# Kernel optimization log

Hardware: AMD Instinct MI355X
Metric: run time of the kernel (lower is better)

Reference implementation:

```python
import jax, jax.numpy as jnp
import numpy as np

MAX_W, MIN_W = 120, 24


def setup_inputs() -> dict:
    key = jax.random.key(0)
    ks = jax.random.split(key, 11)
    B, S, D, H = 2, 2048, 1024, 16
    hd = D // H
    s = 1.0 / float(np.sqrt(D))
    return {
        "x": jax.random.normal(ks[0], (B, S, D), jnp.float32),
        "alpha": jnp.float32(0.1),
        "Wq": jax.random.normal(ks[1], (D, D), jnp.float32) * s,
        "bq": jnp.zeros((D,), jnp.float32),
        "Wk": jax.random.normal(ks[2], (D, D), jnp.float32) * s,
        "bk": jnp.zeros((D,), jnp.float32),
        "Wv": jax.random.normal(ks[3], (D, D), jnp.float32) * s,
        "bv": jnp.zeros((D,), jnp.float32),
        "W_o": jax.random.normal(ks[4], (H, hd, hd), jnp.float32),
        "Wfc": jax.random.normal(ks[5], (D, D), jnp.float32) * s,
        "bfc": jnp.zeros((D,), jnp.float32),
    }


def reference(x, alpha, Wq, bq, Wk, bk, Wv, bv, W_o, Wfc, bfc):
    B, S, D = x.shape
    H, hd, _ = W_o.shape
    # --- dynamic window size (step==0 path of the module) ---
    fluct = jnp.abs(x[:, -1] - x[:, -2])            # [B, D]
    a = jax.nn.sigmoid(alpha)
    ewma_prev = fluct[0, 0]                          # step==0: ewma_prev = fluct_step_value
    signal = a * fluct.mean() + (1.0 - a) * ewma_prev
    scale = jax.nn.sigmoid(signal)
    w = jnp.floor(MIN_W + (MAX_W - MIN_W) * scale).astype(jnp.int32)  # int() truncation
    half = w // 2
    # --- projections ---
    q = (x @ Wq + bq).reshape(B, S, H, hd).transpose(0, 2, 1, 3)  # [B,H,S,hd]
    k = (x @ Wk + bk).reshape(B, S, H, hd).transpose(0, 2, 1, 3)
    v = (x @ Wv + bv).reshape(B, S, H, hd).transpose(0, 2, 1, 3)
    inv_sqrt = 1.0 / float(np.sqrt(hd))
    scores = jnp.einsum('bhqd,bhkd->bhqk', q, k) * inv_sqrt       # [B,H,S,S]
    # banded window mask: allowed iff i - w//2 <= j <= i + w//2
    idx = jnp.arange(S)
    band = jnp.abs(idx[:, None] - idx[None, :]) <= half            # [S,S]
    scores = jnp.where(band[None, None], scores, -1e30)
    attn = jax.nn.softmax(scores, axis=-1)
    out = jnp.einsum('bhqk,bhkd->bhqd', attn, v)                   # [B,H,S,hd]
    out = jnp.einsum('bhqd,hdk->bhqk', out, W_o)                   # per-head output matmul
    out = out.transpose(0, 2, 1, 3).reshape(B, S, D)
    return out @ Wfc + bfc
```

## Files before the change

### kernel.cpp

```cpp
#include <hip/hip_runtime.h>
#include <hip/hip_bf16.h>
#include <stdint.h>
#include <stddef.h>

#define S_LEN 2048
#define DMODEL 1024
#define NHEAD 16
#define HDIM 64
#define BATCH 2
#define MROWS (BATCH * S_LEN)
#define QKV_LD 3072

typedef unsigned short u16;
typedef __attribute__((ext_vector_type(8))) short bf16x8;
typedef __attribute__((ext_vector_type(4))) float f32x4;

__device__ inline u16 f32_to_bf16(float f) {
  union { float f; unsigned int u; } v; v.f = f;
  unsigned int u = v.u;
  unsigned int r = (u + 0x7fffu + ((u >> 16) & 1u)) >> 16;
  return (u16)r;
}

__device__ inline void gload16(const u16* g, u16* l) {
  __builtin_amdgcn_global_load_lds(
      (const __attribute__((address_space(1))) unsigned int*)g,
      (__attribute__((address_space(3))) unsigned int*)l, 16, 0, 0);
}

__global__ __launch_bounds__(256) void conv_x_bf16(const float* __restrict__ x,
                                                   u16* __restrict__ xb,
                                                   const float* __restrict__ alpha,
                                                   int* __restrict__ halfw) {
  if (blockIdx.x == 2048) {
    __shared__ float red[4];
    int tid = threadIdx.x;
    float s = 0.f;
    for (int i = tid; i < BATCH * DMODEL; i += 256) {
      int b = i >> 10, d = i & 1023;
      size_t base = (size_t)b * S_LEN * DMODEL + d;
      float f1 = x[base + (size_t)(S_LEN - 1) * DMODEL];
      float f0 = x[base + (size_t)(S_LEN - 2) * DMODEL];
      s += fabsf(f1 - f0);
    }
#pragma unroll
    for (int m = 32; m >= 1; m >>= 1) s += __shfl_xor(s, m, 64);
    if ((tid & 63) == 0) red[tid >> 6] = s;
    __syncthreads();
    if (tid == 0) {
      float total = red[0] + red[1] + red[2] + red[3];
      float mean = total / (float)(BATCH * DMODEL);
      float e1 = x[(size_t)(S_LEN - 1) * DMODEL];
      float e0 = x[(size_t)(S_LEN - 2) * DMODEL];
      float ew = fabsf(e1 - e0);
      float a = 1.f / (1.f + expf(-alpha[0]));
      float sig = a * mean + (1.f - a) * ew;
      float scale = 1.f / (1.f + expf(-sig));
      int wv = (int)floorf(24.f + 96.f * scale);
      *halfw = wv >> 1;
    }
    return;
  }
  size_t i = ((size_t)blockIdx.x * 256 + threadIdx.x) * 8;
  float4 v0 = *(const float4*)(x + i);
  float4 v1 = *(const float4*)(x + i + 4);
  bf16x8 r;
  r[0] = (short)f32_to_bf16(v0.x); r[1] = (short)f32_to_bf16(v0.y);
  r[2] = (short)f32_to_bf16(v0.z); r[3] = (short)f32_to_bf16(v0.w);
  r[4] = (short)f32_to_bf16(v1.x); r[5] = (short)f32_to_bf16(v1.y);
  r[6] = (short)f32_to_bf16(v1.z); r[7] = (short)f32_to_bf16(v1.w);
  *(bf16x8*)(xb + i) = r;
}

__global__ __launch_bounds__(256) void transpose_qkv(const float* __restrict__ Wq,
                                                     const float* __restrict__ Wk,
                                                     const float* __restrict__ Wv,
                                                     u16* __restrict__ Wt) {
  __shared__ float tile[32][33];
  const float* W = blockIdx.z == 0 ? Wq : (blockIdx.z == 1 ? Wk : Wv);
  int k0 = blockIdx.x * 32, n0 = blockIdx.y * 32;
  int tx = threadIdx.x, ty = threadIdx.y;
#pragma unroll
  for (int i = 0; i < 4; ++i)
    tile[ty + i * 8][tx] = W[(size_t)(k0 + ty + i * 8) * DMODEL + n0 + tx];
  __syncthreads();
  u16* o = Wt + (size_t)blockIdx.z * DMODEL * DMODEL;
#pragma unroll
  for (int i = 0; i < 4; ++i)
    o[(size_t)(n0 + ty + i * 8) * DMODEL + k0 + tx] = f32_to_bf16(tile[tx][ty + i * 8]);
}

__global__ __launch_bounds__(128) void build_wc(const float* __restrict__ W_o,
                                                const float* __restrict__ Wfc,
                                                u16* __restrict__ Wc_t) {
  __shared__ float lds[64 * 128];
  int nb = blockIdx.x, h = blockIdx.y, tx = threadIdx.x;
  int n0 = nb * 128;
#pragma unroll
  for (int c = 0; c < 64; ++c)
    lds[c * 128 + tx] = Wfc[(size_t)(h * 64 + c) * DMODEL + n0 + tx];
  __syncthreads();
  float acc[64];
#pragma unroll
  for (int d = 0; d < 64; ++d) acc[d] = 0.f;
  for (int c = 0; c < 64; ++c) {
    float wv = lds[c * 128 + tx];
#pragma unroll
    for (int d = 0; d < 64; ++d)
      acc[d] += W_o[(size_t)(h * 64 + d) * 64 + c] * wv;
  }
  u16 tmp[64];
#pragma unroll
  for (int d = 0; d < 64; ++d) tmp[d] = f32_to_bf16(acc[d]);
  u16* dst = Wc_t + (size_t)(n0 + tx) * DMODEL + h * 64;
#pragma unroll
  for (int q = 0; q < 8; ++q)
    *(bf16x8*)(dst + q * 8) = *(bf16x8*)(tmp + q * 8);
}

#define G1_BM 256
#define G1_BN 192
#define G1_ASZ (G1_BM * 64)
#define G1_BSZ (G1_BN * 64)
__global__ __launch_bounds__(512, 2) void gemm_qkv(
    const u16* __restrict__ A, const u16* __restrict__ Bt,
    const float* __restrict__ bq, const float* __restrict__ bk,
    const float* __restrict__ bv, u16* __restrict__ out) {
  __shared__ __align__(16) u16 smem[2][G1_ASZ + G1_BSZ];

  const int tid = threadIdx.x;
  const int l = tid & 63, w = tid >> 6;
  const int wr = w >> 2, wc = w & 3;
  const int lrow = l & 15, lk = l >> 4;

  const int xcd = blockIdx.x & 7;
  const int idx = blockIdx.x >> 3;
  const int bm = idx & 15;
  const int bn = xcd * 2 + (idx >> 4);
  const int rowA0 = bm * G1_BM;
  const int colB0 = bn * G1_BN;

  f32x4 acc[8][3] = {};

  auto stage = [&](int buf, int kt) {
    u16* As = smem[buf];
    u16* Bs = smem[buf] + G1_ASZ;
#pragma unroll
    for (int i = 0; i < 4; ++i) {
      int c = i * 512 + tid;
      int row = c >> 3, u = c & 7;
      const u16* g = A + (size_t)(rowA0 + row) * DMODEL + kt + ((u ^ (row & 7)) << 3);
      gload16(g, As + c * 8);
    }
#pragma unroll
    for (int i = 0; i < 3; ++i) {
      int c = i * 512 + tid;
      int row = c >> 3, u = c & 7;
      const u16* g = Bt + (size_t)(colB0 + row) * DMODEL + kt + ((u ^ (row & 7)) << 3);
      gload16(g, Bs + c * 8);
    }
  };

  stage(0, 0);
  asm volatile("s_waitcnt vmcnt(0)");
  __syncthreads();

  int buf = 0;
#pragma unroll 1
  for (int t = 0; t < 16; ++t) {
    if (t < 15) stage(buf ^ 1, (t + 1) * 64);
    const u16* As = smem[buf];
    const u16* Bs = smem[buf] + G1_ASZ;
#pragma unroll
    for (int kk = 0; kk < 2; ++kk) {
      bf16x8 af[8], bg[3];
      const int ksw = ((kk << 2) + lk);
#pragma unroll
      for (int m = 0; m < 8; ++m) {
        int r = wr * 128 + m * 16 + lrow;
        af[m] = *(const bf16x8*)(As + r * 64 + ((ksw ^ (lrow & 7)) << 3));
      }
#pragma unroll
      for (int n = 0; n < 3; ++n) {
        int r = wc * 48 + n * 16 + lrow;
        bg[n] = *(const bf16x8*)(Bs + r * 64 + ((ksw ^ (lrow & 7)) << 3));
      }
#pragma unroll
      for (int m = 0; m < 8; ++m)
#pragma unroll
        for (int n = 0; n < 3; ++n)
          acc[m][n] = __builtin_amdgcn_mfma_f32_16x16x32_bf16(af[m], bg[n], acc[m][n], 0, 0, 0);
    }
    if (t < 15) {
      asm volatile("s_waitcnt vmcnt(0)");
      __syncthreads();
      buf ^= 1;
    }
  }

#pragma unroll
  for (int n = 0; n < 3; ++n) {
    int c = colB0 + wc * 48 + n * 16 + lrow;
    float bias = (c < 1024) ? bq[c] : ((c < 2048) ? bk[c - 1024] : bv[c - 2048]);
    float mult = (c < 1024) ? 0.125f : 1.0f;
#pragma unroll
    for (int m = 0; m < 8; ++m) {
      int r0 = rowA0 + wr * 128 + m * 16 + lk * 4;
#pragma unroll
      for (int j = 0; j < 4; ++j)
        out[(size_t)(r0 + j) * QKV_LD + c] = f32_to_bf16((acc[m][n][j] + bias) * mult);
    }
  }
}

__global__ __launch_bounds__(256) void gemm_fc(const u16* __restrict__ A,
                                               const u16* __restrict__ Bt,
                                               const float* __restrict__ bias,
                                               float* __restrict__ out) {
  __shared__ __align__(16) u16 smem[2][256 * 64];

  const int tid = threadIdx.x;
  const int l = tid & 63, w = tid >> 6;
  const int wr = w >> 1, wc = w & 1;
  const int lrow = l & 15, lk = l >> 4;

  const int bn = blockIdx.x & 7;
  const int bm = blockIdx.x >> 3;
  const int rowA0 = bm * 128, colB0 = bn * 128;

  f32x4 acc[4][4] = {};

  auto stage = [&](int buf, int kt) {
    u16* As = smem[buf];
    u16* Bs = smem[buf] + 128 * 64;
#pragma unroll
    for (int i = 0; i < 4; ++i) {
      int c = i * 256 + tid;
      int row = c >> 3, u = c & 7;
      const u16* g = A + (size_t)(rowA0 + row) * DMODEL + kt + ((u ^ (row & 7)) << 3);
      gload16(g, As + c * 8);
    }
#pragma unroll
    for (int i = 0; i < 4; ++i) {
      int c = i * 256 + tid;
      int row = c >> 3, u = c & 7;
      const u16* g = Bt + (size_t)(colB0 + row) * DMODEL + kt + ((u ^ (row & 7)) << 3);
      gload16(g, Bs + c * 8);
    }
  };

  stage(0, 0);
  asm volatile("s_waitcnt vmcnt(0)");
  __syncthreads();

  int buf = 0;
#pragma unroll 1
  for (int t = 0; t < 16; ++t) {
    if (t < 15) stage(buf ^ 1, (t + 1) * 64);
    const u16* As = smem[buf];
    const u16* Bs = smem[buf] + 128 * 64;
#pragma unroll
    for (int kk = 0; kk < 2; ++kk) {
      bf16x8 af[4], bg[4];
      const int ksw = ((kk << 2) + lk);
#pragma unroll
      for (int m = 0; m < 4; ++m) {
        int r = wr * 64 + m * 16 + lrow;
        af[m] = *(const bf16x8*)(As + r * 64 + ((ksw ^ (lrow & 7)) << 3));
      }
#pragma unroll
      for (int n = 0; n < 4; ++n) {
        int r = wc * 64 + n * 16 + lrow;
        bg[n] = *(const bf16x8*)(Bs + r * 64 + ((ksw ^ (lrow & 7)) << 3));
      }
#pragma unroll
      for (int m = 0; m < 4; ++m)
#pragma unroll
        for (int n = 0; n < 4; ++n)
          acc[m][n] = __builtin_amdgcn_mfma_f32_16x16x32_bf16(af[m], bg[n], acc[m][n], 0, 0, 0);
    }
    if (t < 15) {
      asm volatile("s_waitcnt vmcnt(0)");
      __syncthreads();
      buf ^= 1;
    }
  }

#pragma unroll
  for (int n = 0; n < 4; ++n) {
    int c = colB0 + wc * 64 + n * 16 + lrow;
    float bv = bias[c];
#pragma unroll
    for (int m = 0; m < 4; ++m) {
      int r0 = rowA0 + wr * 64 + m * 16 + lk * 4;
#pragma unroll
      for (int j = 0; j < 4; ++j)
        out[(size_t)(r0 + j) * DMODEL + c] = acc[m][n][j] + bv;
    }
  }
}

__global__ __launch_bounds__(256) void attn_win(const u16* __restrict__ qkv,
                                                u16* __restrict__ ao,
                                                const int* __restrict__ halfptr) {
  __shared__ __align__(16) u16 KP[12800];
  __shared__ __align__(16) u16 Vt[64 * 200];
  const int tid = threadIdx.x, l = tid & 63, w = tid >> 6;
  const int lrow = l & 15, lk = l >> 4;
  const int q0 = blockIdx.x * 64, k0 = q0 - 64;
  const int h = blockIdx.y, b = blockIdx.z;
  const int halfw = *halfptr;

  const u16* qb = qkv;
  const u16* kb = qkv + 1024;
  const u16* vb = qkv + 2048;

#pragma unroll
  for (int i = 0; i < 6; ++i) {
    int c = i * 256 + tid;
    int row = c >> 3, u = c & 7;
    const u16* g = kb + (ptrdiff_t)((b * S_LEN + k0 + row) * QKV_LD + h * 64 + ((u ^ (row & 7)) << 3));
    gload16(g, KP + c * 8);
  }
  const int qrow = q0 + w * 16 + lrow;
  bf16x8 qf[2];
#pragma unroll
  for (int kk = 0; kk < 2; ++kk)
    qf[kk] = *(const bf16x8*)(qb + (ptrdiff_t)((b * S_LEN + qrow) * QKV_LD + h * 64 + kk * 32 + lk * 8));
  bf16x8 vreg[6];
#pragma unroll
  for (int i = 0; i < 6; ++i) {
    int c = i * 256 + tid;
    int row = c % 192, ch = c / 192;
    vreg[i] = *(const bf16x8*)(vb + (ptrdiff_t)((b * S_LEN + k0 + row) * QKV_LD + h * 64 + ch * 8));
  }

  asm volatile("s_waitcnt vmcnt(0)" ::: "memory");
  __syncthreads();

  f32x4 sc[12];
#pragma unroll
  for (int f = 0; f < 12; ++f) sc[f] = (f32x4){0.f, 0.f, 0.f, 0.f};
#pragma unroll
  for (int kk = 0; kk < 2; ++kk) {
#pragma unroll
    for (int f = 0; f < 12; ++f) {
      bf16x8 kf = *(const bf16x8*)(KP + (f * 16 + lrow) * 64 + ((((kk << 2) + lk) ^ (lrow & 7)) << 3));
      sc[f] = __builtin_amdgcn_mfma_f32_16x16x32_bf16(qf[kk], kf, sc[f], 0, 0, 0);
    }
  }

#pragma unroll
  for (int i = 0; i < 6; ++i) {
    int c = i * 256 + tid;
    int row = c % 192, ch = c / 192;
#pragma unroll
    for (int e = 0; e < 8; ++e)
      Vt[(ch * 8 + e) * 200 + row] = (u16)vreg[i][e];
  }

  float rmax[4] = {-3e38f, -3e38f, -3e38f, -3e38f};
  const int qbase = q0 + w * 16 + lk * 4;
#pragma unroll
  for (int f = 0; f < 12; ++f) {
    int kj = k0 + f * 16 + lrow;
    bool kok = (kj >= 0) && (kj < S_LEN);
#pragma unroll
    for (int j = 0; j < 4; ++j) {
      int qi = qbase + j;
      float v = sc[f][j];
      int dd = qi - kj;
      int ad = dd < 0 ? -dd : dd;
      v = (kok && ad <= halfw) ? v : -1e30f;
      sc[f][j] = v;
      rmax[j] = fmaxf(rmax[j], v);
    }
  }
#pragma unroll
  for (int j = 0; j < 4; ++j) {
    rmax[j] = fmaxf(rmax[j], __shfl_xor(rmax[j], 1, 16));
    rmax[j] = fmaxf(rmax[j], __shfl_xor(rmax[j], 2, 16));
    rmax[j] = fmaxf(rmax[j], __shfl_xor(rmax[j], 4, 16));
    rmax[j] = fmaxf(rmax[j], __shfl_xor(rmax[j], 8, 16));
  }
  float rsum[4] = {0.f, 0.f, 0.f, 0.f};
#pragma unroll
  for (int f = 0; f < 12; ++f)
#pragma unroll
    for (int j = 0; j < 4; ++j) {
      float e = __expf(sc[f][j] - rmax[j]);
      sc[f][j] = e;
      rsum[j] += e;
    }
#pragma unroll
  for (int j = 0; j < 4; ++j) {
    rsum[j] += __shfl_xor(rsum[j], 1, 16);
    rsum[j] += __shfl_xor(rsum[j], 2, 16);
    rsum[j] += __shfl_xor(rsum[j], 4, 16);
    rsum[j] += __shfl_xor(rsum[j], 8, 16);
  }
  float rinv[4];
#pragma unroll
  for (int j = 0; j < 4; ++j) rinv[j] = 1.0f / rsum[j];

  __syncthreads();

  u16* Ps = KP;
#pragma unroll
  for (int f = 0; f < 12; ++f)
#pragma unroll
    for (int j = 0; j < 4; ++j) {
      int prow = w * 16 + lk * 4 + j;
      Ps[prow * 200 + f * 16 + lrow] = f32_to_bf16(sc[f][j] * rinv[j]);
    }
  __syncthreads();

  f32x4 o[4] = {};
#pragma unroll
  for (int jt = 0; jt < 6; ++jt) {
    bf16x8 pa = *(const bf16x8*)(Ps + (w * 16 + lrow) * 200 + jt * 32 + lk * 8);
#pragma unroll
    for (int n = 0; n < 4; ++n) {
      bf16x8 vf = *(const bf16x8*)(Vt + (n * 16 + lrow) * 200 + jt * 32 + lk * 8);
      o[n] = __builtin_amdgcn_mfma_f32_16x16x32_bf16(pa, vf, o[n], 0, 0, 0);
    }
  }
#pragma unroll
  for (int n = 0; n < 4; ++n)
#pragma unroll
    for (int j = 0; j < 4; ++j) {
      int qi = q0 + w * 16 + lk * 4 + j;
      int d = n * 16 + lrow;
      ao[(size_t)(b * S_LEN + qi) * DMODEL + h * 64 + d] = f32_to_bf16(o[n][j]);
    }
}

extern "C" void kernel_launch(void* const* d_in, const int* in_sizes, int n_in,
                              void* d_out, int out_size, void* d_ws, size_t ws_size,
                              hipStream_t stream) {
  (void)in_sizes; (void)n_in; (void)out_size; (void)ws_size;
  const float* x     = (const float*)d_in[0];
  const float* alpha = (const float*)d_in[1];
  const float* Wq    = (const float*)d_in[2];
  const float* bq    = (const float*)d_in[3];
  const float* Wk    = (const float*)d_in[4];
  const float* bk    = (const float*)d_in[5];
  const float* Wv    = (const float*)d_in[6];
  const float* bv    = (const float*)d_in[7];
  const float* W_o   = (const float*)d_in[8];
  const float* Wfc   = (const float*)d_in[9];
  const float* bfc   = (const float*)d_in[10];

  char* ws = (char*)d_ws;
  int* halfw  = (int*)ws;
  u16* xb     = (u16*)(ws + 256);
  u16* Wqkv_t = xb + (size_t)MROWS * DMODEL;
  u16* qkv    = Wqkv_t + (size_t)3 * DMODEL * DMODEL;
  u16* ao     = qkv + (size_t)MROWS * QKV_LD;
  u16* Wc_t   = ao + (size_t)MROWS * DMODEL;

  hipLaunchKernelGGL(conv_x_bf16, dim3(MROWS * DMODEL / (256 * 8) + 1), dim3(256), 0, stream,
                     x, xb, alpha, halfw);
  hipLaunchKernelGGL(transpose_qkv, dim3(32, 32, 3), dim3(32, 8), 0, stream, Wq, Wk, Wv, Wqkv_t);
  hipLaunchKernelGGL(build_wc, dim3(8, 16), dim3(128), 0, stream, W_o, Wfc, Wc_t);
  hipLaunchKernelGGL(gemm_qkv, dim3(256), dim3(512), 0, stream,
                     xb, Wqkv_t, bq, bk, bv, qkv);
  hipLaunchKernelGGL(attn_win, dim3(S_LEN / 64, NHEAD, BATCH), dim3(256), 0, stream,
                     qkv, ao, halfw);
  hipLaunchKernelGGL(gemm_fc, dim3(256), dim3(256), 0, stream,
                     ao, Wc_t, bfc, (float*)d_out);
}
```

Measured before the change: 104.5 us.

## Merge prep kernels into one launch and overlap loads with MFMA in GEMMs

```diff
diff --git a/kernel.cpp b/kernel.cpp
--- a/kernel.cpp
+++ b/kernel.cpp
@@ -28,13 +28,26 @@
       (__attribute__((address_space(3))) unsigned int*)l, 16, 0, 0);
 }
 
-__global__ __launch_bounds__(256) void conv_x_bf16(const float* __restrict__ x,
-                                                   u16* __restrict__ xb,
-                                                   const float* __restrict__ alpha,
-                                                   int* __restrict__ halfw) {
-  if (blockIdx.x == 2048) {
-    __shared__ float red[4];
-    int tid = threadIdx.x;
+__global__ __launch_bounds__(256) void prep(const float* __restrict__ x, u16* __restrict__ xb,
+                                            const float* __restrict__ alpha, int* __restrict__ halfw,
+                                            const float* __restrict__ Wq, const float* __restrict__ Wk,
+                                            const float* __restrict__ Wv, u16* __restrict__ Wt,
+                                            const float* __restrict__ W_o, const float* __restrict__ Wfc,
+                                            u16* __restrict__ Wc_t) {
+  __shared__ float lds[64 * 256];
+  const int bid = blockIdx.x, tid = threadIdx.x;
+
+  if (bid < 2048) {
+    size_t i = ((size_t)bid * 256 + tid) * 8;
+    float4 v0 = *(const float4*)(x + i);
+    float4 v1 = *(const float4*)(x + i + 4);
+    bf16x8 r;
+    r[0] = (short)f32_to_bf16(v0.x); r[1] = (short)f32_to_bf16(v0.y);
+    r[2] = (short)f32_to_bf16(v0.z); r[3] = (short)f32_to_bf16(v0.w);
+    r[4] = (short)f32_to_bf16(v1.x); r[5] = (short)f32_to_bf16(v1.y);
+    r[6] = (short)f32_to_bf16(v1.z); r[7] = (short)f32_to_bf16(v1.w);
+    *(bf16x8*)(xb + i) = r;
+  } else if (bid == 2048) {
     float s = 0.f;
     for (int i = tid; i < BATCH * DMODEL; i += 256) {
       int b = i >> 10, d = i & 1023;
@@ -45,10 +58,10 @@
     }
 #pragma unroll
     for (int m = 32; m >= 1; m >>= 1) s += __shfl_xor(s, m, 64);
-    if ((tid & 63) == 0) red[tid >> 6] = s;
+    if ((tid & 63) == 0) lds[tid >> 6] = s;
     __syncthreads();
     if (tid == 0) {
-      float total = red[0] + red[1] + red[2] + red[3];
+      float total = lds[0] + lds[1] + lds[2] + lds[3];
       float mean = total / (float)(BATCH * DMODEL);
       float e1 = x[(size_t)(S_LEN - 1) * DMODEL];
       float e0 = x[(size_t)(S_LEN - 2) * DMODEL];
@@ -59,69 +72,50 @@
       int wv = (int)floorf(24.f + 96.f * scale);
       *halfw = wv >> 1;
     }
-    return;
-  }
-  size_t i = ((size_t)blockIdx.x * 256 + threadIdx.x) * 8;
-  float4 v0 = *(const float4*)(x + i);
-  float4 v1 = *(const float4*)(x + i + 4);
-  bf16x8 r;
-  r[0] = (short)f32_to_bf16(v0.x); r[1] = (short)f32_to_bf16(v0.y);
-  r[2] = (short)f32_to_bf16(v0.z); r[3] = (short)f32_to_bf16(v0.w);
-  r[4] = (short)f32_to_bf16(v1.x); r[5] = (short)f32_to_bf16(v1.y);
-  r[6] = (short)f32_to_bf16(v1.z); r[7] = (short)f32_to_bf16(v1.w);
-  *(bf16x8*)(xb + i) = r;
-}
-
-__global__ __launch_bounds__(256) void transpose_qkv(const float* __restrict__ Wq,
-                                                     const float* __restrict__ Wk,
-                                                     const float* __restrict__ Wv,
-                                                     u16* __restrict__ Wt) {
-  __shared__ float tile[32][33];
-  const float* W = blockIdx.z == 0 ? Wq : (blockIdx.z == 1 ? Wk : Wv);
-  int k0 = blockIdx.x * 32, n0 = blockIdx.y * 32;
-  int tx = threadIdx.x, ty = threadIdx.y;
-#pragma unroll
-  for (int i = 0; i < 4; ++i)
-    tile[ty + i * 8][tx] = W[(size_t)(k0 + ty + i * 8) * DMODEL + n0 + tx];
-  __syncthreads();
-  u16* o = Wt + (size_t)blockIdx.z * DMODEL * DMODEL;
-#pragma unroll
-  for (int i = 0; i < 4; ++i)
-    o[(size_t)(n0 + ty + i * 8) * DMODEL + k0 + tx] = f32_to_bf16(tile[tx][ty + i * 8]);
-}
-
-__global__ __launch_bounds__(128) void build_wc(const float* __restrict__ W_o,
-                                                const float* __restrict__ Wfc,
-                                                u16* __restrict__ Wc_t) {
-  __shared__ float lds[64 * 128];
-  int nb = blockIdx.x, h = blockIdx.y, tx = threadIdx.x;
-  int n0 = nb * 128;
-#pragma unroll
-  for (int c = 0; c < 64; ++c)
-    lds[c * 128 + tx] = Wfc[(size_t)(h * 64 + c) * DMODEL + n0 + tx];
-  __syncthreads();
-  float acc[64];
-#pragma unroll
-  for (int d = 0; d < 64; ++d) acc[d] = 0.f;
-  for (int c = 0; c < 64; ++c) {
-    float wv = lds[c * 128 + tx];
-#pragma unroll
-    for (int d = 0; d < 64; ++d)
-      acc[d] += W_o[(size_t)(h * 64 + d) * 64 + c] * wv;
-  }
-  u16 tmp[64];
-#pragma unroll
-  for (int d = 0; d < 64; ++d) tmp[d] = f32_to_bf16(acc[d]);
-  u16* dst = Wc_t + (size_t)(n0 + tx) * DMODEL + h * 64;
-#pragma unroll
-  for (int q = 0; q < 8; ++q)
-    *(bf16x8*)(dst + q * 8) = *(bf16x8*)(tmp + q * 8);
-}
-
-#define G1_BM 256
-#define G1_BN 192
-#define G1_ASZ (G1_BM * 64)
-#define G1_BSZ (G1_BN * 64)
+  } else if (bid < 2049 + 3072) {
+    float (*tile)[33] = (float (*)[33])lds;
+    const int r = bid - 2049;
+    const int z = r >> 10, rem = r & 1023;
+    const int k0 = (rem >> 5) * 32, n0 = (rem & 31) * 32;
+    const float* W = z == 0 ? Wq : (z == 1 ? Wk : Wv);
+    const int tx = tid & 31, ty = tid >> 5;
+#pragma unroll
+    for (int i = 0; i < 4; ++i)
+      tile[ty + i * 8][tx] = W[(size_t)(k0 + ty + i * 8) * DMODEL + n0 + tx];
+    __syncthreads();
+    u16* o = Wt + (size_t)z * DMODEL * DMODEL;
+#pragma unroll
+    for (int i = 0; i < 4; ++i)
+      o[(size_t)(n0 + ty + i * 8) * DMODEL + k0 + tx] = f32_to_bf16(tile[tx][ty + i * 8]);
+  } else {
+    const int idx = bid - 5121;
+    const int nb = idx & 3, h = idx >> 2;
+    const int n0 = nb * 256;
+#pragma unroll
+    for (int c = 0; c < 64; ++c)
+      lds[c * 256 + tid] = Wfc[(size_t)(h * 64 + c) * DMODEL + n0 + tid];
+    __syncthreads();
+    float acc[64];
+#pragma unroll
+    for (int d = 0; d < 64; ++d) acc[d] = 0.f;
+    for (int c = 0; c < 64; ++c) {
+      float wv = lds[c * 256 + tid];
+#pragma unroll
+      for (int d = 0; d < 64; ++d)
+        acc[d] += W_o[(size_t)(h * 64 + d) * 64 + c] * wv;
+    }
+    u16 tmp[64];
+#pragma unroll
+    for (int d = 0; d < 64; ++d) tmp[d] = f32_to_bf16(acc[d]);
+    u16* dst = Wc_t + (size_t)(n0 + tid) * DMODEL + h * 64;
+#pragma unroll
+    for (int q = 0; q < 8; ++q)
+      *(bf16x8*)(dst + q * 8) = *(bf16x8*)(tmp + q * 8);
+  }
+}
+
+#define G1_ASZ (256 * 64)
+#define G1_BSZ (192 * 64)
 __global__ __launch_bounds__(512, 2) void gemm_qkv(
     const u16* __restrict__ A, const u16* __restrict__ Bt,
     const float* __restrict__ bq, const float* __restrict__ bk,
@@ -137,8 +131,8 @@
   const int idx = blockIdx.x >> 3;
   const int bm = idx & 15;
   const int bn = xcd * 2 + (idx >> 4);
-  const int rowA0 = bm * G1_BM;
-  const int colB0 = bn * G1_BN;
+  const int rowA0 = bm * 256;
+  const int colB0 = bn * 192;
 
   f32x4 acc[8][3] = {};
 
@@ -162,40 +156,52 @@
   };
 
   stage(0, 0);
-  asm volatile("s_waitcnt vmcnt(0)");
-  __syncthreads();
 
   int buf = 0;
 #pragma unroll 1
   for (int t = 0; t < 16; ++t) {
-    if (t < 15) stage(buf ^ 1, (t + 1) * 64);
+    if (t < 15) {
+      stage(buf ^ 1, (t + 1) * 64);
+      asm volatile("s_waitcnt vmcnt(7)" ::: "memory");
+    } else {
+      asm volatile("s_waitcnt vmcnt(0)" ::: "memory");
+    }
+    __builtin_amdgcn_s_barrier();
+    asm volatile("" ::: "memory");
+
     const u16* As = smem[buf];
     const u16* Bs = smem[buf] + G1_ASZ;
 #pragma unroll
     for (int kk = 0; kk < 2; ++kk) {
-      bf16x8 af[8], bg[3];
       const int ksw = ((kk << 2) + lk);
-#pragma unroll
-      for (int m = 0; m < 8; ++m) {
-        int r = wr * 128 + m * 16 + lrow;
-        af[m] = *(const bf16x8*)(As + r * 64 + ((ksw ^ (lrow & 7)) << 3));
-      }
+      const int swz = ((ksw ^ (lrow & 7)) << 3);
+      bf16x8 bg[3];
 #pragma unroll
       for (int n = 0; n < 3; ++n) {
         int r = wc * 48 + n * 16 + lrow;
-        bg[n] = *(const bf16x8*)(Bs + r * 64 + ((ksw ^ (lrow & 7)) << 3));
+        bg[n] = *(const bf16x8*)(Bs + r * 64 + swz);
       }
 #pragma unroll
-      for (int m = 0; m < 8; ++m)
-#pragma unroll
-        for (int n = 0; n < 3; ++n)
-          acc[m][n] = __builtin_amdgcn_mfma_f32_16x16x32_bf16(af[m], bg[n], acc[m][n], 0, 0, 0);
-    }
-    if (t < 15) {
-      asm volatile("s_waitcnt vmcnt(0)");
-      __syncthreads();
-      buf ^= 1;
-    }
+      for (int mh = 0; mh < 2; ++mh) {
+        bf16x8 af[4];
+#pragma unroll
+        for (int i = 0; i < 4; ++i) {
+          int r = wr * 128 + (mh * 4 + i) * 16 + lrow;
+          af[i] = *(const bf16x8*)(As + r * 64 + swz);
+        }
+        __builtin_amdgcn_s_setprio(1);
+#pragma unroll
+        for (int i = 0; i < 4; ++i)
+#pragma unroll
+          for (int n = 0; n < 3; ++n)
+            acc[mh * 4 + i][n] =
+                __builtin_amdgcn_mfma_f32_16x16x32_bf16(af[i], bg[n], acc[mh * 4 + i][n], 0, 0, 0);
+        __builtin_amdgcn_s_setprio(0);
+        __builtin_amdgcn_s_barrier();
+      }
+    }
+    asm volatile("" ::: "memory");
+    buf ^= 1;
   }
 
 #pragma unroll
@@ -250,40 +256,46 @@
   };
 
   stage(0, 0);
-  asm volatile("s_waitcnt vmcnt(0)");
-  __syncthreads();
 
   int buf = 0;
 #pragma unroll 1
   for (int t = 0; t < 16; ++t) {
-    if (t < 15) stage(buf ^ 1, (t + 1) * 64);
+    if (t < 15) {
+      stage(buf ^ 1, (t + 1) * 64);
+      asm volatile("s_waitcnt vmcnt(8)" ::: "memory");
+    } else {
+      asm volatile("s_waitcnt vmcnt(0)" ::: "memory");
+    }
+    __builtin_amdgcn_s_barrier();
+    asm volatile("" ::: "memory");
+
     const u16* As = smem[buf];
     const u16* Bs = smem[buf] + 128 * 64;
 #pragma unroll
     for (int kk = 0; kk < 2; ++kk) {
+      const int swz = ((((kk << 2) + lk) ^ (lrow & 7)) << 3);
       bf16x8 af[4], bg[4];
-      const int ksw = ((kk << 2) + lk);
 #pragma unroll
       for (int m = 0; m < 4; ++m) {
         int r = wr * 64 + m * 16 + lrow;
-        af[m] = *(const bf16x8*)(As + r * 64 + ((ksw ^ (lrow & 7)) << 3));
+        af[m] = *(const bf16x8*)(As + r * 64 + swz);
       }
 #pragma unroll
       for (int n = 0; n < 4; ++n) {
         int r = wc * 64 + n * 16 + lrow;
-        bg[n] = *(const bf16x8*)(Bs + r * 64 + ((ksw ^ (lrow & 7)) << 3));
+        bg[n] = *(const bf16x8*)(Bs + r * 64 + swz);
       }
+      __builtin_amdgcn_s_setprio(1);
 #pragma unroll
       for (int m = 0; m < 4; ++m)
 #pragma unroll
         for (int n = 0; n < 4; ++n)
           acc[m][n] = __builtin_amdgcn_mfma_f32_16x16x32_bf16(af[m], bg[n], acc[m][n], 0, 0, 0);
-    }
-    if (t < 15) {
-      asm volatile("s_waitcnt vmcnt(0)");
-      __syncthreads();
-      buf ^= 1;
-    }
+      __builtin_amdgcn_s_setprio(0);
+      __builtin_amdgcn_s_barrier();
+    }
+    asm volatile("" ::: "memory");
+    buf ^= 1;
   }
 
 #pragma unroll
@@ -459,10 +471,8 @@
   u16* ao     = qkv + (size_t)MROWS * QKV_LD;
   u16* Wc_t   = ao + (size_t)MROWS * DMODEL;
 
-  hipLaunchKernelGGL(conv_x_bf16, dim3(MROWS * DMODEL / (256 * 8) + 1), dim3(256), 0, stream,
-                     x, xb, alpha, halfw);
-  hipLaunchKernelGGL(transpose_qkv, dim3(32, 32, 3), dim3(32, 8), 0, stream, Wq, Wk, Wv, Wqkv_t);
-  hipLaunchKernelGGL(build_wc, dim3(8, 16), dim3(128), 0, stream, W_o, Wfc, Wc_t);
+  hipLaunchKernelGGL(prep, dim3(5185), dim3(256), 0, stream,
+                     x, xb, alpha, halfw, Wq, Wk, Wv, Wqkv_t, W_o, Wfc, Wc_t);
   hipLaunchKernelGGL(gemm_qkv, dim3(256), dim3(512), 0, stream,
                      xb, Wqkv_t, bq, bk, bv, qkv);
   hipLaunchKernelGGL(attn_win, dim3(S_LEN / 64, NHEAD, BATCH), dim3(256), 0, stream,
```

New measurement: 118.3 us. 1.13x slower.
